# Optimization experiments

Measured on AMD Instinct MI355X. Metric: run time of the kernel, lower is better.

## Reference

```python
import jax, jax.numpy as jnp
import numpy as np

N_NODES = 1_000_000   # rows in the feature table
N_TARGETS = 100_000   # target nodes being aggregated
NUM_SAMPLES = 32      # neighbors sampled per node (with replacement)
D = 128               # in_channels == out_channels for mean aggregation


def setup_inputs() -> dict:
    key = jax.random.key(0)
    k1, k2 = jax.random.split(key)
    features = jax.random.normal(k1, (N_NODES, D), dtype=jnp.float32)
    # Pre-sampled neighbor indices (replaces per-node np.random.choice loop;
    # sampling with replacement yields a fixed-width [n, num_samples] matrix).
    neighbor_idx = jax.random.randint(k2, (N_TARGETS, NUM_SAMPLES), 0, N_NODES, dtype=jnp.int64)
    return {"features": features, "neighbor_idx": neighbor_idx}


def reference(features, neighbor_idx):
    # Fused gather + segment mean: out[i] = mean_j features[neighbor_idx[i, j]]
    gathered = jnp.take(features, neighbor_idx, axis=0)   # [n, num_samples, D]
    return jnp.mean(gathered, axis=1)                     # [n, D]
```

## Files before the change

### kernel.cpp

```cpp
#include <hip/hip_runtime.h>


constexpr int D = 128;
constexpr int S = 32;
constexpr int D2 = D / 2;

__global__ __launch_bounds__(256) void Aggregator_20710332301461_kernel(
    const float* __restrict__ feat,
    const int* __restrict__ idx,
    float* __restrict__ out,
    int n_targets)
{
    const int lane = threadIdx.x & 63;
    const int wave_in_block = threadIdx.x >> 6;
    const int waves_per_block = blockDim.x >> 6;
    const int wave_global = blockIdx.x * waves_per_block + wave_in_block;
    const int n_waves = gridDim.x * waves_per_block;

    const float2* __restrict__ f2 = reinterpret_cast<const float2*>(feat);
    float2* __restrict__ o2 = reinterpret_cast<float2*>(out);

    for (int t = wave_global; t < n_targets; t += n_waves) {
        int myidx = 0;
        if (lane < S) myidx = idx[t * S + lane];

        float ax = 0.f, ay = 0.f;
        #pragma unroll
        for (int j = 0; j < S; ++j) {
            int r = __shfl(myidx, j);
            float2 v = f2[(long)r * D2 + lane];
            ax += v.x;
            ay += v.y;
        }
        float2 res;
        res.x = ax * (1.f / S);
        res.y = ay * (1.f / S);
        o2[(long)t * D2 + lane] = res;
    }
}

extern "C" void kernel_launch(void* const* d_in, const int* in_sizes, int n_in,
                              void* d_out, int out_size, void* d_ws, size_t ws_size,
                              hipStream_t stream) {
    const float* feat = (const float*)d_in[0];
    const int* idx = (const int*)d_in[1];
    float* out = (float*)d_out;

    const int n_targets = out_size / D;

    const int block = 256;
    const int waves_per_block = block / 64;
    int grid = (n_targets + waves_per_block - 1) / waves_per_block;
    if (grid > 2048) grid = 2048;

    Aggregator_20710332301461_kernel<<<grid, block, 0, stream>>>(feat, idx, out, n_targets);
}
```

Measured before the change: 245.6 us.

## Partition gathers into row-range phases across many targets per wave for cache locality

Each wave now owns up to 13 targets (strided by 8192 waves) and holds their indices and accumulators in registers. Gathers run in four phases, each restricted to one quarter of the feature-table rows (by index bits above 18), so the working set in each phase is smaller and more likely to stay in L2/MALL cache. The costs are extra register pressure, divergent predicated loads, repeated shuffles across phases, and a hardcoded 8192-wave grid. Targets beyond 13×8192 would be skipped.

After: 727.9 us. 2.96x slower.

```diff
diff --git a/kernel.cpp b/kernel.cpp
--- a/kernel.cpp
+++ b/kernel.cpp
@@ -4,6 +4,10 @@
 constexpr int D = 128;
 constexpr int S = 32;
 constexpr int D2 = D / 2;
+constexpr int T = 13;
+constexpr int NPHASE = 4;
+constexpr int PH_SHIFT = 18;
+constexpr int N_WAVES = 8192;
 
 __global__ __launch_bounds__(256) void Aggregator_20710332301461_kernel(
     const float* __restrict__ feat,
@@ -12,30 +16,48 @@
     int n_targets)
 {
     const int lane = threadIdx.x & 63;
-    const int wave_in_block = threadIdx.x >> 6;
-    const int waves_per_block = blockDim.x >> 6;
-    const int wave_global = blockIdx.x * waves_per_block + wave_in_block;
-    const int n_waves = gridDim.x * waves_per_block;
+    const int w = blockIdx.x * (blockDim.x >> 6) + (threadIdx.x >> 6);
 
     const float2* __restrict__ f2 = reinterpret_cast<const float2*>(feat);
     float2* __restrict__ o2 = reinterpret_cast<float2*>(out);
 
-    for (int t = wave_global; t < n_targets; t += n_waves) {
-        int myidx = 0;
-        if (lane < S) myidx = idx[t * S + lane];
+    int myidx[T];
+    float ax[T], ay[T];
+    #pragma unroll
+    for (int k = 0; k < T; ++k) {
+        const int t = w + k * N_WAVES;
+        myidx[k] = 0;
+        ax[k] = 0.f;
+        ay[k] = 0.f;
+        if (t < n_targets && lane < S) myidx[k] = idx[t * S + lane];
+    }
 
-        float ax = 0.f, ay = 0.f;
+    for (int ph = 0; ph < NPHASE; ++ph) {
         #pragma unroll
-        for (int j = 0; j < S; ++j) {
-            int r = __shfl(myidx, j);
-            float2 v = f2[(long)r * D2 + lane];
-            ax += v.x;
-            ay += v.y;
+        for (int k = 0; k < T; ++k) {
+            const int t = w + k * N_WAVES;
+            if (t >= n_targets) continue;
+            #pragma unroll 8
+            for (int j = 0; j < S; ++j) {
+                const int r = __shfl(myidx[k], j);
+                if ((r >> PH_SHIFT) == ph) {
+                    const float2 v = f2[(size_t)r * D2 + lane];
+                    ax[k] += v.x;
+                    ay[k] += v.y;
+                }
+            }
         }
-        float2 res;
-        res.x = ax * (1.f / S);
-        res.y = ay * (1.f / S);
-        o2[(long)t * D2 + lane] = res;
+    }
+
+    #pragma unroll
+    for (int k = 0; k < T; ++k) {
+        const int t = w + k * N_WAVES;
+        if (t < n_targets) {
+            float2 res;
+            res.x = ax[k] * (1.f / S);
+            res.y = ay[k] * (1.f / S);
+            o2[(size_t)t * D2 + lane] = res;
+        }
     }
 }
 
@@ -49,9 +71,7 @@
     const int n_targets = out_size / D;
 
     const int block = 256;
-    const int waves_per_block = block / 64;
-    int grid = (n_targets + waves_per_block - 1) / waves_per_block;
-    if (grid > 2048) grid = 2048;
+    const int grid = N_WAVES / (block / 64);
 
     Aggregator_20710332301461_kernel<<<grid, block, 0, stream>>>(feat, idx, out, n_targets);
 }
```
